# Optimization experiments

Measured on AMD Instinct MI355X. Metric: run time of the kernel, lower is better.

## Reference

```python
import jax, jax.numpy as jnp
import numpy as np

H = 128      # hidden_size
P = 50000    # num_predicates
C = 20000    # num_clauses
K = 3        # clause_size (3-SAT)
B = 4        # batch
SAT_ITERS = 2


def setup_inputs() -> dict:
    key = jax.random.key(0)
    ks = jax.random.split(key, 10)
    s = 0.02
    return {
        "clause_indices": jax.random.randint(ks[0], (B, C, K), 0, P),
        "variable_states": jax.random.normal(ks[1], (B, P, H), jnp.float32),
        "W_vc": jax.random.normal(ks[2], (H, H), jnp.float32) * s,
        "b_vc": jnp.zeros((H,), jnp.float32),
        "W_ce": jax.random.normal(ks[3], (H, H), jnp.float32) * s,
        "b_ce": jnp.zeros((H,), jnp.float32),
        "W_cv": jax.random.normal(ks[4], (H, H), jnp.float32) * s,
        "b_cv": jnp.zeros((H,), jnp.float32),
        "W_s1": jax.random.normal(ks[5], (H, H), jnp.float32) * s,
        "b_s1": jnp.zeros((H,), jnp.float32),
        "W_s2": jax.random.normal(ks[6], (1, H), jnp.float32) * s,
        "b_s2": jnp.zeros((1,), jnp.float32),
    }


def _forward(clause_indices, variable_states,
             W_vc, b_vc, W_ce, b_ce, W_cv, b_cv, W_s1, b_s1, W_s2, b_s2):
    Bn, Cn, Kn = clause_indices.shape
    Pn = variable_states.shape[1]
    # first-occurrence mask within each clause: duplicates of a variable inside
    # one clause must contribute once ((clause_indices == v).any(-1) semantics).
    eq = clause_indices[..., :, None] == clause_indices[..., None, :]  # [B,C,K,K]
    first = ~jnp.any(jnp.tril(eq, -1), axis=-1)                        # [B,C,K]
    w = first.reshape(-1).astype(variable_states.dtype)                # [B*C*K]
    flat_idx = clause_indices.reshape(-1)                              # [B*C*K]
    counts = jax.ops.segment_sum(w, flat_idx, num_segments=Pn)        # [P]
    batch_ix = jnp.arange(Bn)[:, None, None]

    for _ in range(SAT_ITERS):
        # clause side: gather -> var_to_clause -> mean over clause -> clause_embedding
        gathered = variable_states[batch_ix, clause_indices]           # [B,C,K,H]
        cv = jnp.einsum('bckh,oh->bcko', gathered, W_vc) + b_vc        # [B,C,K,H]
        clause_states = jnp.einsum('bch,oh->bco', cv.mean(2), W_ce) + b_ce  # [B,C,H]
        # variable side: per-variable mean of clause_to_var over all (b, c)
        # where the variable appears; message broadcast across batch.
        M = jnp.einsum('bch,oh->bco', clause_states, W_cv) + b_cv      # [B,C,H]
        Mflat = jnp.broadcast_to(M[:, :, None, :], (Bn, Cn, Kn, M.shape[-1])).reshape(-1, M.shape[-1])
        sums = jax.ops.segment_sum(Mflat * w[:, None], flat_idx, num_segments=Pn)  # [P,H]
        msgs = jnp.where(counts[:, None] > 0,
                         sums / jnp.maximum(counts, 1.0)[:, None],
                         0.0)                                          # [P,H]
        variable_states = variable_states + msgs[None]                 # broadcast over batch

    h = jax.nn.relu(jnp.einsum('bph,oh->bpo', variable_states, W_s1) + b_s1)
    logits = jnp.einsum('bph,oh->bpo', h, W_s2) + b_s2                 # [B,P,1]
    return jax.nn.sigmoid(logits)[..., 0]                              # [B,P]


def reference(clause_indices, variable_states,
              W_vc, b_vc, W_ce, b_ce, W_cv, b_cv, W_s1, b_s1, W_s2, b_s2):
    return _forward(clause_indices, variable_states,
                    W_vc, b_vc, W_ce, b_ce, W_cv, b_cv, W_s1, b_s1, W_s2, b_s2)
```

## Files before the change

kernel.cpp:

```cpp
#include <hip/hip_runtime.h>
#include <math.h>

using u16 = unsigned short;
using u32 = unsigned int;

namespace {
constexpr int Hdim = 128;
constexpr int Pn = 50000;
constexpr int Cn = 20000;
constexpr int Bn = 4;
constexpr int NClause = Bn * Cn;
constexpr int NRows = Bn * Pn;
constexpr int CAP = 64;
}

typedef __attribute__((ext_vector_type(4))) float f32x4;
typedef __attribute__((ext_vector_type(8))) short bf16x8;

static __device__ __forceinline__ float bf2f(u16 v) {
    u32 u = ((u32)v) << 16;
    return __builtin_bit_cast(float, u);
}
static __device__ __forceinline__ u16 f2bf(float f) {
    u32 u = __builtin_bit_cast(u32, f);
    u32 r = u + 0x7FFFu + ((u >> 16) & 1u);
    return (u16)(r >> 16);
}

__global__ __launch_bounds__(128) void setup_kernel(
    const float* __restrict__ W_vc, const float* __restrict__ b_vc,
    const float* __restrict__ W_ce, const float* __restrict__ b_ce,
    const float* __restrict__ W_cv, const float* __restrict__ b_cv,
    const float* __restrict__ W_s1,
    u16* __restrict__ WcombPack, u16* __restrict__ Ws1Pack,
    float* __restrict__ bias_comb, int* __restrict__ cursor) {
    int o = blockIdx.x, t = threadIdx.x;
    __shared__ float u[Hdim];
    __shared__ float red[Hdim];
    float acc = 0.f;
#pragma unroll 8
    for (int h = 0; h < Hdim; ++h) acc = fmaf(W_cv[o * Hdim + h], W_ce[h * Hdim + t], acc);
    u[t] = acc;
    float b1 = b_ce[t];
#pragma unroll 8
    for (int h = 0; h < Hdim; ++h) b1 = fmaf(W_ce[t * Hdim + h], b_vc[h], b1);
    red[t] = W_cv[o * Hdim + t] * b1;
    __syncthreads();
#pragma unroll
    for (int s = 64; s > 0; s >>= 1) {
        if (t < s) red[t] += red[t + s];
        __syncthreads();
    }
    if (t == 0) bias_comb[o] = red[0] + b_cv[o];
    float w = 0.f;
#pragma unroll 8
    for (int h = 0; h < Hdim; ++h) w = fmaf(u[h], W_vc[h * Hdim + t], w);
    int nt = o >> 4, ks = t >> 5, lofs = (t >> 3) & 3, j = t & 7;
    int lane = lofs * 16 + (o & 15);
    size_t dst = (size_t)(((nt * 4 + ks) * 64 + lane)) * 8 + j;
    WcombPack[dst] = f2bf(w);
    Ws1Pack[dst] = f2bf(W_s1[o * Hdim + t]);
    for (int i = o * 128 + t; i < Pn; i += 128 * 128) cursor[i] = 0;
}

__global__ void fill_kernel(const int* __restrict__ ci, int* __restrict__ cursor,
                            int* __restrict__ entries) {
    int fid = blockIdx.x * blockDim.x + threadIdx.x;
    if (fid >= NClause) return;
    int i0 = ci[fid * 3 + 0], i1 = ci[fid * 3 + 1], i2 = ci[fid * 3 + 2];
    int pos = atomicAdd(&cursor[i0], 1);
    entries[i0 * CAP + pos] = fid;
    if (i1 != i0) { pos = atomicAdd(&cursor[i1], 1); entries[i1 * CAP + pos] = fid; }
    if (i2 != i0 && i2 != i1) { pos = atomicAdd(&cursor[i2], 1); entries[i2 * CAP + pos] = fid; }
}

template <int FROM_F32>
__global__ __launch_bounds__(256) void clause_kernel(
    const int* __restrict__ ci, const float* __restrict__ vs0, const u16* __restrict__ msgs,
    const u16* __restrict__ Bpack, const float* __restrict__ bias, u16* __restrict__ M) {
    __shared__ __align__(16) u16 Atile[64 * 136];
    __shared__ __align__(16) u16 Btile[128 * 128];
    int tid = threadIdx.x;
    int block0 = blockIdx.x * 64;
    {
        const bf16x8* s = (const bf16x8*)Bpack;
        bf16x8* d = (bf16x8*)Btile;
#pragma unroll
        for (int i = 0; i < 8; ++i) d[tid + i * 256] = s[tid + i * 256];
    }
#pragma unroll
    for (int pass = 0; pass < 4; ++pass) {
        int t = pass * 256 + tid;
        int r = t >> 4, seg = t & 15;
        int fid = block0 + r;
        int i0 = ci[fid * 3 + 0], i1 = ci[fid * 3 + 1], i2 = ci[fid * 3 + 2];
        int co = seg * 8;
        float s[8];
        if (FROM_F32) {
            const float* base = vs0 + (size_t)(fid / Cn) * Pn * Hdim;
            const float* r0 = base + (size_t)i0 * Hdim + co;
            const float* r1 = base + (size_t)i1 * Hdim + co;
            const float* r2 = base + (size_t)i2 * Hdim + co;
            f32x4 a0 = *(const f32x4*)r0, a1 = *(const f32x4*)(r0 + 4);
            f32x4 b0 = *(const f32x4*)r1, b1 = *(const f32x4*)(r1 + 4);
            f32x4 c0 = *(const f32x4*)r2, c1 = *(const f32x4*)(r2 + 4);
#pragma unroll
            for (int j = 0; j < 4; ++j) {
                s[j] = a0[j] + b0[j] + c0[j];
                s[j + 4] = a1[j] + b1[j] + c1[j];
            }
        } else {
            bf16x8 v0 = *(const bf16x8*)(msgs + (size_t)i0 * Hdim + co);
            bf16x8 v1 = *(const bf16x8*)(msgs + (size_t)i1 * Hdim + co);
            bf16x8 v2 = *(const bf16x8*)(msgs + (size_t)i2 * Hdim + co);
#pragma unroll
            for (int j = 0; j < 8; ++j)
                s[j] = bf2f((u16)v0[j]) + bf2f((u16)v1[j]) + bf2f((u16)v2[j]);
        }
        bf16x8 o;
#pragma unroll
        for (int j = 0; j < 8; ++j) o[j] = (short)f2bf(s[j] * (1.f / 3.f));
        *(bf16x8*)(&Atile[r * 136 + seg * 8]) = o;
    }
    __syncthreads();
    int w = tid >> 6, l = tid & 63;
    int arow = w * 16 + (l & 15);
    int kofs = (l >> 4) * 8;
    f32x4 acc[8];
#pragma unroll
    for (int nt = 0; nt < 8; ++nt) acc[nt] = (f32x4){0.f, 0.f, 0.f, 0.f};
#pragma unroll
    for (int ks = 0; ks < 4; ++ks) {
        bf16x8 af = *(const bf16x8*)(&Atile[arow * 136 + ks * 32 + kofs]);
#pragma unroll
        for (int nt = 0; nt < 8; ++nt) {
            bf16x8 bfr = *(const bf16x8*)(&Btile[((nt * 4 + ks) * 64 + l) * 8]);
            acc[nt] = __builtin_amdgcn_mfma_f32_16x16x32_bf16(af, bfr, acc[nt], 0, 0, 0);
        }
    }
    __syncthreads();
    int crow = w * 16 + (l >> 4) * 4;
#pragma unroll
    for (int nt = 0; nt < 8; ++nt) {
        int col = nt * 16 + (l & 15);
        float bc = FROM_F32 ? bias[col] : 0.f;
#pragma unroll
        for (int reg = 0; reg < 4; ++reg)
            Atile[(crow + reg) * 136 + col] = f2bf(acc[nt][reg] + bc);
    }
    __syncthreads();
#pragma unroll
    for (int pass = 0; pass < 4; ++pass) {
        int t = pass * 256 + tid;
        int r = t >> 4, seg = t & 15;
        *(bf16x8*)(M + (size_t)(block0 + r) * Hdim + seg * 8) =
            *(const bf16x8*)(&Atile[r * 136 + seg * 8]);
    }
}

__global__ __launch_bounds__(256) void var_kernel(const u16* __restrict__ M,
                                                  const int* __restrict__ counts,
                                                  const int* __restrict__ entries,
                                                  u16* __restrict__ msgs, int iter2) {
    int wave = threadIdx.x >> 6, lane = threadIdx.x & 63;
    int p = blockIdx.x * 4 + wave;
    if (p >= Pn) return;
    int deg = counts[p];
    const int* ep = entries + p * CAP;
    float a0 = 0.f, a1 = 0.f;
    for (int e = 0; e < deg; ++e) {
        int cid = ep[e];
        u32 v = *(const u32*)(M + (size_t)cid * Hdim + lane * 2);
        a0 += bf2f((u16)(v & 0xffffu));
        a1 += bf2f((u16)(v >> 16));
    }
    if (deg > 0) { float inv = 1.f / (float)deg; a0 *= inv; a1 *= inv; }
    u32* mp = (u32*)(msgs + (size_t)p * Hdim + lane * 2);
    if (iter2) {
        u32 old = *mp;
        a0 += 2.f * bf2f((u16)(old & 0xffffu));
        a1 += 2.f * bf2f((u16)(old >> 16));
    }
    *mp = (u32)f2bf(a0) | ((u32)f2bf(a1) << 16);
}

__global__ __launch_bounds__(256) void final_kernel(
    const float* __restrict__ vs0, const u16* __restrict__ msgs, const u16* __restrict__ Bpack,
    const float* __restrict__ b_s1, const float* __restrict__ W_s2, const float* __restrict__ b_s2,
    float* __restrict__ out) {
    __shared__ __align__(16) u16 Atile[64 * 136];
    __shared__ __align__(16) u16 Btile[128 * 128];
    int tid = threadIdx.x;
    int block0 = blockIdx.x * 64;
    {
        const bf16x8* s = (const bf16x8*)Bpack;
        bf16x8* d = (bf16x8*)Btile;
#pragma unroll
        for (int i = 0; i < 8; ++i) d[tid + i * 256] = s[tid + i * 256];
    }
#pragma unroll
    for (int pass = 0; pass < 4; ++pass) {
        int t = pass * 256 + tid;
        int r = t >> 4, seg = t & 15;
        int row = block0 + r;
        int p = row % Pn;
        int co = seg * 8;
        const float* vp = vs0 + (size_t)row * Hdim + co;
        f32x4 x = *(const f32x4*)vp, y = *(const f32x4*)(vp + 4);
        bf16x8 m = *(const bf16x8*)(msgs + (size_t)p * Hdim + co);
        bf16x8 o;
#pragma unroll
        for (int j = 0; j < 4; ++j) {
            o[j] = (short)f2bf(x[j] + bf2f((u16)m[j]));
            o[j + 4] = (short)f2bf(y[j] + bf2f((u16)m[j + 4]));
        }
        *(bf16x8*)(&Atile[r * 136 + seg * 8]) = o;
    }
    __syncthreads();
    int w = tid >> 6, l = tid & 63;
    int arow = w * 16 + (l & 15);
    int kofs = (l >> 4) * 8;
    f32x4 acc[8];
#pragma unroll
    for (int nt = 0; nt < 8; ++nt) acc[nt] = (f32x4){0.f, 0.f, 0.f, 0.f};
#pragma unroll
    for (int ks = 0; ks < 4; ++ks) {
        bf16x8 af = *(const bf16x8*)(&Atile[arow * 136 + ks * 32 + kofs]);
#pragma unroll
        for (int nt = 0; nt < 8; ++nt) {
            bf16x8 bfr = *(const bf16x8*)(&Btile[((nt * 4 + ks) * 64 + l) * 8]);
            acc[nt] = __builtin_amdgcn_mfma_f32_16x16x32_bf16(af, bfr, acc[nt], 0, 0, 0);
        }
    }
    float part[4] = {0.f, 0.f, 0.f, 0.f};
#pragma unroll
    for (int nt = 0; nt < 8; ++nt) {
        int col = nt * 16 + (l & 15);
        float b1 = b_s1[col], w2 = W_s2[col];
#pragma unroll
        for (int reg = 0; reg < 4; ++reg)
            part[reg] += fmaxf(acc[nt][reg] + b1, 0.f) * w2;
    }
#pragma unroll
    for (int m = 1; m < 16; m <<= 1)
#pragma unroll
        for (int reg = 0; reg < 4; ++reg) part[reg] += __shfl_xor(part[reg], m, 64);
    if ((l & 15) == 0) {
        float lb = b_s2[0];
        int row0 = block0 + w * 16 + (l >> 4) * 4;
#pragma unroll
        for (int reg = 0; reg < 4; ++reg)
            out[row0 + reg] = 1.f / (1.f + expf(-(part[reg] + lb)));
    }
}

extern "C" void kernel_launch(void* const* d_in, const int* in_sizes, int n_in,
                              void* d_out, int out_size, void* d_ws, size_t ws_size,
                              hipStream_t stream) {
    (void)in_sizes; (void)n_in; (void)out_size; (void)ws_size;
    const int* ci = (const int*)d_in[0];
    const float* vs0 = (const float*)d_in[1];
    const float* W_vc = (const float*)d_in[2];
    const float* b_vc = (const float*)d_in[3];
    const float* W_ce = (const float*)d_in[4];
    const float* b_ce = (const float*)d_in[5];
    const float* W_cv = (const float*)d_in[6];
    const float* b_cv = (const float*)d_in[7];
    const float* W_s1 = (const float*)d_in[8];
    const float* b_s1 = (const float*)d_in[9];
    const float* W_s2 = (const float*)d_in[10];
    const float* b_s2 = (const float*)d_in[11];
    float* out = (float*)d_out;

    char* ws = (char*)d_ws;
    size_t off = 0;
    auto alloc = [&](size_t bytes) -> void* {
        off = (off + 255) & ~(size_t)255;
        void* p = ws + off;
        off += bytes;
        return p;
    };
    float* bias_comb = (float*)alloc(Hdim * 4);
    u16* WcombPack = (u16*)alloc(Hdim * Hdim * 2);
    u16* Ws1Pack = (u16*)alloc(Hdim * Hdim * 2);
    int* cursor = (int*)alloc(Pn * 4);
    int* entries = (int*)alloc((size_t)Pn * CAP * 4);
    u16* M = (u16*)alloc((size_t)NClause * Hdim * 2);
    u16* msgs = (u16*)alloc((size_t)Pn * Hdim * 2);

    setup_kernel<<<Hdim, Hdim, 0, stream>>>(W_vc, b_vc, W_ce, b_ce, W_cv, b_cv, W_s1,
                                            WcombPack, Ws1Pack, bias_comb, cursor);
    fill_kernel<<<(NClause + 255) / 256, 256, 0, stream>>>(ci, cursor, entries);

    clause_kernel<1><<<NClause / 64, 256, 0, stream>>>(ci, vs0, nullptr, WcombPack, bias_comb, M);
    var_kernel<<<(Pn + 3) / 4, 256, 0, stream>>>(M, cursor, entries, msgs, 0);
    clause_kernel<0><<<NClause / 64, 256, 0, stream>>>(ci, nullptr, msgs, WcombPack, bias_comb, M);
    var_kernel<<<(Pn + 3) / 4, 256, 0, stream>>>(M, cursor, entries, msgs, 1);
    final_kernel<<<NRows / 64, 256, 0, stream>>>(vs0, msgs, Ws1Pack, b_s1, W_s2, b_s2, out);
}
```

Measured before the change: 159.5 us.

## Build MFMA A-fragments directly from global gathers and use 128-row blocks

The clause and final kernels no longer stage the gathered or summed input rows in an LDS A-tile. Each lane now loads its own 8-element slice for each k-step from global memory and converts it straight into the MFMA A operand. Blocks grow to 512 threads covering 128 rows, so the 32 KB weight tile is loaded into LDS once per 128 rows instead of once per 64. This removes one LDS round trip and a barrier. In exchange, each lane issues more scattered global loads that are not coalesced across a row, and the final kernel needs clamping for the partial last block.

```diff
diff --git a/kernel.cpp b/kernel.cpp
--- a/kernel.cpp
+++ b/kernel.cpp
@@ -75,32 +75,36 @@
 }
 
 template <int FROM_F32>
-__global__ __launch_bounds__(256) void clause_kernel(
+__global__ __launch_bounds__(512) void clause_kernel(
     const int* __restrict__ ci, const float* __restrict__ vs0, const u16* __restrict__ msgs,
     const u16* __restrict__ Bpack, const float* __restrict__ bias, u16* __restrict__ M) {
-    __shared__ __align__(16) u16 Atile[64 * 136];
     __shared__ __align__(16) u16 Btile[128 * 128];
+    __shared__ __align__(16) u16 Otile[128 * 136];
     int tid = threadIdx.x;
-    int block0 = blockIdx.x * 64;
+    int block0 = blockIdx.x * 128;
     {
         const bf16x8* s = (const bf16x8*)Bpack;
         bf16x8* d = (bf16x8*)Btile;
 #pragma unroll
-        for (int i = 0; i < 8; ++i) d[tid + i * 256] = s[tid + i * 256];
-    }
-#pragma unroll
-    for (int pass = 0; pass < 4; ++pass) {
-        int t = pass * 256 + tid;
-        int r = t >> 4, seg = t & 15;
-        int fid = block0 + r;
-        int i0 = ci[fid * 3 + 0], i1 = ci[fid * 3 + 1], i2 = ci[fid * 3 + 2];
-        int co = seg * 8;
+        for (int i = 0; i < 4; ++i) d[tid + i * 512] = s[tid + i * 512];
+    }
+    __syncthreads();
+    int w = tid >> 6, l = tid & 63;
+    int fid = block0 + w * 16 + (l & 15);
+    int kofs = (l >> 4) * 8;
+    int i0 = ci[fid * 3 + 0], i1 = ci[fid * 3 + 1], i2 = ci[fid * 3 + 2];
+    f32x4 acc[8];
+#pragma unroll
+    for (int nt = 0; nt < 8; ++nt) acc[nt] = (f32x4){0.f, 0.f, 0.f, 0.f};
+    const float* fb = FROM_F32 ? vs0 + (size_t)(fid / Cn) * Pn * Hdim : nullptr;
+#pragma unroll
+    for (int ks = 0; ks < 4; ++ks) {
+        int co = ks * 32 + kofs;
         float s[8];
         if (FROM_F32) {
-            const float* base = vs0 + (size_t)(fid / Cn) * Pn * Hdim;
-            const float* r0 = base + (size_t)i0 * Hdim + co;
-            const float* r1 = base + (size_t)i1 * Hdim + co;
-            const float* r2 = base + (size_t)i2 * Hdim + co;
+            const float* r0 = fb + (size_t)i0 * Hdim + co;
+            const float* r1 = fb + (size_t)i1 * Hdim + co;
+            const float* r2 = fb + (size_t)i2 * Hdim + co;
             f32x4 a0 = *(const f32x4*)r0, a1 = *(const f32x4*)(r0 + 4);
             f32x4 b0 = *(const f32x4*)r1, b1 = *(const f32x4*)(r1 + 4);
             f32x4 c0 = *(const f32x4*)r2, c1 = *(const f32x4*)(r2 + 4);
@@ -117,28 +121,15 @@
             for (int j = 0; j < 8; ++j)
                 s[j] = bf2f((u16)v0[j]) + bf2f((u16)v1[j]) + bf2f((u16)v2[j]);
         }
-        bf16x8 o;
-#pragma unroll
-        for (int j = 0; j < 8; ++j) o[j] = (short)f2bf(s[j] * (1.f / 3.f));
-        *(bf16x8*)(&Atile[r * 136 + seg * 8]) = o;
-    }
-    __syncthreads();
-    int w = tid >> 6, l = tid & 63;
-    int arow = w * 16 + (l & 15);
-    int kofs = (l >> 4) * 8;
-    f32x4 acc[8];
-#pragma unroll
-    for (int nt = 0; nt < 8; ++nt) acc[nt] = (f32x4){0.f, 0.f, 0.f, 0.f};
-#pragma unroll
-    for (int ks = 0; ks < 4; ++ks) {
-        bf16x8 af = *(const bf16x8*)(&Atile[arow * 136 + ks * 32 + kofs]);
+        bf16x8 af;
+#pragma unroll
+        for (int j = 0; j < 8; ++j) af[j] = (short)f2bf(s[j] * (1.f / 3.f));
 #pragma unroll
         for (int nt = 0; nt < 8; ++nt) {
             bf16x8 bfr = *(const bf16x8*)(&Btile[((nt * 4 + ks) * 64 + l) * 8]);
             acc[nt] = __builtin_amdgcn_mfma_f32_16x16x32_bf16(af, bfr, acc[nt], 0, 0, 0);
         }
     }
-    __syncthreads();
     int crow = w * 16 + (l >> 4) * 4;
 #pragma unroll
     for (int nt = 0; nt < 8; ++nt) {
@@ -146,15 +137,15 @@
         float bc = FROM_F32 ? bias[col] : 0.f;
 #pragma unroll
         for (int reg = 0; reg < 4; ++reg)
-            Atile[(crow + reg) * 136 + col] = f2bf(acc[nt][reg] + bc);
+            Otile[(crow + reg) * 136 + col] = f2bf(acc[nt][reg] + bc);
     }
     __syncthreads();
 #pragma unroll
     for (int pass = 0; pass < 4; ++pass) {
-        int t = pass * 256 + tid;
+        int t = pass * 512 + tid;
         int r = t >> 4, seg = t & 15;
         *(bf16x8*)(M + (size_t)(block0 + r) * Hdim + seg * 8) =
-            *(const bf16x8*)(&Atile[r * 136 + seg * 8]);
+            *(const bf16x8*)(&Otile[r * 136 + seg * 8]);
     }
 }
 
@@ -184,48 +175,41 @@
     *mp = (u32)f2bf(a0) | ((u32)f2bf(a1) << 16);
 }
 
-__global__ __launch_bounds__(256) void final_kernel(
+__global__ __launch_bounds__(512) void final_kernel(
     const float* __restrict__ vs0, const u16* __restrict__ msgs, const u16* __restrict__ Bpack,
     const float* __restrict__ b_s1, const float* __restrict__ W_s2, const float* __restrict__ b_s2,
     float* __restrict__ out) {
-    __shared__ __align__(16) u16 Atile[64 * 136];
     __shared__ __align__(16) u16 Btile[128 * 128];
     int tid = threadIdx.x;
-    int block0 = blockIdx.x * 64;
+    int block0 = blockIdx.x * 128;
     {
         const bf16x8* s = (const bf16x8*)Bpack;
         bf16x8* d = (bf16x8*)Btile;
 #pragma unroll
-        for (int i = 0; i < 8; ++i) d[tid + i * 256] = s[tid + i * 256];
-    }
-#pragma unroll
-    for (int pass = 0; pass < 4; ++pass) {
-        int t = pass * 256 + tid;
-        int r = t >> 4, seg = t & 15;
-        int row = block0 + r;
-        int p = row % Pn;
-        int co = seg * 8;
-        const float* vp = vs0 + (size_t)row * Hdim + co;
-        f32x4 x = *(const f32x4*)vp, y = *(const f32x4*)(vp + 4);
-        bf16x8 m = *(const bf16x8*)(msgs + (size_t)p * Hdim + co);
-        bf16x8 o;
+        for (int i = 0; i < 4; ++i) d[tid + i * 512] = s[tid + i * 512];
+    }
+    __syncthreads();
+    int w = tid >> 6, l = tid & 63;
+    int row = block0 + w * 16 + (l & 15);
+    int rowc = row < NRows ? row : NRows - 1;
+    int p = rowc % Pn;
+    int kofs = (l >> 4) * 8;
+    const float* vrow = vs0 + (size_t)rowc * Hdim;
+    const u16* mrow = msgs + (size_t)p * Hdim;
+    f32x4 acc[8];
+#pragma unroll
+    for (int nt = 0; nt < 8; ++nt) acc[nt] = (f32x4){0.f, 0.f, 0.f, 0.f};
+#pragma unroll
+    for (int ks = 0; ks < 4; ++ks) {
+        int co = ks * 32 + kofs;
+        f32x4 x = *(const f32x4*)(vrow + co), y = *(const f32x4*)(vrow + co + 4);
+        bf16x8 m = *(const bf16x8*)(mrow + co);
+        bf16x8 af;
 #pragma unroll
         for (int j = 0; j < 4; ++j) {
-            o[j] = (short)f2bf(x[j] + bf2f((u16)m[j]));
-            o[j + 4] = (short)f2bf(y[j] + bf2f((u16)m[j + 4]));
-        }
-        *(bf16x8*)(&Atile[r * 136 + seg * 8]) = o;
-    }
-    __syncthreads();
-    int w = tid >> 6, l = tid & 63;
-    int arow = w * 16 + (l & 15);
-    int kofs = (l >> 4) * 8;
-    f32x4 acc[8];
-#pragma unroll
-    for (int nt = 0; nt < 8; ++nt) acc[nt] = (f32x4){0.f, 0.f, 0.f, 0.f};
-#pragma unroll
-    for (int ks = 0; ks < 4; ++ks) {
-        bf16x8 af = *(const bf16x8*)(&Atile[arow * 136 + ks * 32 + kofs]);
+            af[j] = (short)f2bf(x[j] + bf2f((u16)m[j]));
+            af[j + 4] = (short)f2bf(y[j] + bf2f((u16)m[j + 4]));
+        }
 #pragma unroll
         for (int nt = 0; nt < 8; ++nt) {
             bf16x8 bfr = *(const bf16x8*)(&Btile[((nt * 4 + ks) * 64 + l) * 8]);
@@ -250,7 +234,8 @@
         int row0 = block0 + w * 16 + (l >> 4) * 4;
 #pragma unroll
         for (int reg = 0; reg < 4; ++reg)
-            out[row0 + reg] = 1.f / (1.f + expf(-(part[reg] + lb)));
+            if (row0 + reg < NRows)
+                out[row0 + reg] = 1.f / (1.f + expf(-(part[reg] + lb)));
     }
 }
 
@@ -292,9 +277,9 @@
                                             WcombPack, Ws1Pack, bias_comb, cursor);
     fill_kernel<<<(NClause + 255) / 256, 256, 0, stream>>>(ci, cursor, entries);
 
-    clause_kernel<1><<<NClause / 64, 256, 0, stream>>>(ci, vs0, nullptr, WcombPack, bias_comb, M);
+    clause_kernel<1><<<NClause / 128, 512, 0, stream>>>(ci, vs0, nullptr, WcombPack, bias_comb, M);
     var_kernel<<<(Pn + 3) / 4, 256, 0, stream>>>(M, cursor, entries, msgs, 0);
-    clause_kernel<0><<<NClause / 64, 256, 0, stream>>>(ci, nullptr, msgs, WcombPack, bias_comb, M);
+    clause_kernel<0><<<NClause / 128, 512, 0, stream>>>(ci, nullptr, msgs, WcombPack, bias_comb, M);
     var_kernel<<<(Pn + 3) / 4, 256, 0, stream>>>(M, cursor, entries, msgs, 1);
-    final_kernel<<<NRows / 64, 256, 0, stream>>>(vs0, msgs, Ws1Pack, b_s1, W_s2, b_s2, out);
-}
+    final_kernel<<<(NRows + 127) / 128, 512, 0, stream>>>(vs0, msgs, Ws1Pack, b_s1, W_s2, b_s2, out);
+}
```

After: 175.9 us. 10.3% more time.
